# Performance work log

Hardware: AMD Instinct MI355X
Metric: run time of the kernel (lower is better)

The kernel has to match this reference:

```python
import jax, jax.numpy as jnp
import numpy as np
import math

D_MODEL = 1024
N_HEADS = 16
HEAD_DIM = D_MODEL // N_HEADS  # 64
KV_DIM = 4 * HEAD_DIM          # 256
THETA = 10000.0
B, T = 2, 2048


def setup_inputs() -> dict:
    key = jax.random.key(0)
    ks = jax.random.split(key, 14)
    s = lambda k, *sh: jax.random.normal(k, sh, dtype=jnp.float32) * 0.02
    inp = {
        "x": jax.random.normal(ks[0], (B, T, D_MODEL), dtype=jnp.float32),
        "mask": jnp.tril(jnp.ones((T, T), dtype=jnp.int32))[None, None],  # causal [1,1,T,T]
        "Wq": s(ks[1], D_MODEL, D_MODEL), "bq": jnp.zeros((D_MODEL,), jnp.float32),
        "Wkv": s(ks[2], D_MODEL, KV_DIM), "bkv": jnp.zeros((KV_DIM,), jnp.float32),
        "Wk": s(ks[3], KV_DIM, D_MODEL), "bk": jnp.zeros((D_MODEL,), jnp.float32),
        "Wv": s(ks[4], KV_DIM, D_MODEL), "bv": jnp.zeros((D_MODEL,), jnp.float32),
        "Wo": s(ks[5], D_MODEL, D_MODEL), "bo": jnp.zeros((D_MODEL,), jnp.float32),
        "Wkr": s(ks[6], HEAD_DIM, HEAD_DIM),  # decoupled k_rope linear, no bias
    }
    return inp


def _rotate_half(x):
    x1, x2 = jnp.split(x, 2, axis=-1)
    return jnp.concatenate((-x2, x1), axis=-1)


def reference(x, mask, Wq, bq, Wkv, bkv, Wk, bk, Wv, bv, Wo, bo, Wkr):
    Bq, Tq, C = x.shape
    kv = x @ Wkv + bkv                                # [B,T,KV_DIM]
    k = (kv @ Wk + bk).reshape(Bq, Tq, N_HEADS, HEAD_DIM).transpose(0, 2, 1, 3)
    v = (kv @ Wv + bv).reshape(Bq, Tq, N_HEADS, HEAD_DIM).transpose(0, 2, 1, 3)
    q = (x @ Wq + bq).reshape(Bq, Tq, N_HEADS, HEAD_DIM).transpose(0, 2, 1, 3)

    # standard RoPE on q
    inv_freq = 1.0 / (THETA ** (jnp.arange(0, HEAD_DIM, 2, dtype=jnp.float32) / HEAD_DIM))
    t = jnp.arange(Tq, dtype=jnp.float32)
    freqs = t[:, None] * inv_freq[None, :]            # [T, D/2]
    emb = jnp.concatenate((freqs, freqs), axis=-1)    # [T, D]
    q = q * jnp.cos(emb) + _rotate_half(q) * jnp.sin(emb)

    # decoupled position path for k: scale by position index, then linear
    k = (k * t[None, None, :, None]) @ Wkr            # [B,H,T,D]

    attn = jnp.einsum('bhtd,bhsd->bhts', q, k) * (1.0 / math.sqrt(HEAD_DIM))
    attn = jnp.where(mask == 0, -jnp.inf, attn)
    attn = jax.nn.softmax(attn, axis=-1)
    y = jnp.einsum('bhts,bhsd->bhtd', attn, v)
    y = y.transpose(0, 2, 1, 3).reshape(Bq, Tq, C)
    return y @ Wo + bo
```

## Files before the change

### kernel.cpp

```cpp
#include <hip/hip_runtime.h>
#include <hip/hip_bf16.h>
#include <math.h>

typedef __bf16 bf16x8 __attribute__((ext_vector_type(8)));
typedef __bf16 bf16x4 __attribute__((ext_vector_type(4)));
typedef float  f32x4  __attribute__((ext_vector_type(4)));

#define T_SEQ 2048
#define NH    16
#define HD    64
#define DM    1024
#define QSCALE 0.18033688011112043f

__device__ __forceinline__ f32x4 mfma16(bf16x8 a, bf16x8 b, f32x4 c) {
    return __builtin_amdgcn_mfma_f32_16x16x32_bf16(a, b, c, 0, 0, 0);
}

__device__ __forceinline__ void tsplit_body(const float* __restrict__ in,
                                            __bf16* __restrict__ oh, __bf16* __restrict__ ol,
                                            int K, int N, int n0, int k0, int SPLIT,
                                            float* tile )
{
    const int tid = threadIdx.x;
#pragma unroll
    for (int it = 0; it < 2; ++it) {
        int r = it * 32 + (tid >> 3), c8 = (tid & 7) * 8;
        f32x4 a0 = *(const f32x4*)&in[(size_t)(k0 + r) * N + n0 + c8];
        f32x4 a1 = *(const f32x4*)&in[(size_t)(k0 + r) * N + n0 + c8 + 4];
#pragma unroll
        for (int j = 0; j < 4; ++j) { tile[r * 65 + c8 + j] = a0[j]; tile[r * 65 + c8 + 4 + j] = a1[j]; }
    }
    __syncthreads();
    const int n = tid >> 2, kb = (tid & 3) * 16;
    bf16x8 h0, h1, l0, l1;
#pragma unroll
    for (int j = 0; j < 8; ++j) {
        float v0 = tile[(kb + j) * 65 + n], v1 = tile[(kb + 8 + j) * 65 + n];
        __bf16 hb0 = (__bf16)v0, hb1 = (__bf16)v1;
        h0[j] = hb0; h1[j] = hb1;
        if (SPLIT) { l0[j] = (__bf16)(v0 - (float)hb0); l1[j] = (__bf16)(v1 - (float)hb1); }
    }
    size_t o = (size_t)(n0 + n) * K + k0 + kb;
    *(bf16x8*)&oh[o] = h0; *(bf16x8*)&oh[o + 8] = h1;
    if (SPLIT) { *(bf16x8*)&ol[o] = l0; *(bf16x8*)&ol[o + 8] = l1; }
}

__global__ __launch_bounds__(256)
void prep(const float* __restrict__ x, const float* __restrict__ Wq,
          const float* __restrict__ Wkv, const float* __restrict__ Wv,
          const float* __restrict__ Wo, const float* __restrict__ Wk,
          const float* __restrict__ Wkr, const float* __restrict__ bk,
          __bf16* xh, __bf16* xl, __bf16* Wqt_h, __bf16* Wqt_l,
          __bf16* Wkvt_h, __bf16* Wkvt_l, __bf16* Wvt, __bf16* Wot,
          __bf16* W2th, __bf16* W2tl, float* b2)
{
    __shared__ float tile[64 * 65];
    const int g = blockIdx.x, tid = threadIdx.x;
    if (g < 2048) {
        size_t idx = ((size_t)g * 256 + tid) * 8;
        f32x4 a0 = *(const f32x4*)&x[idx];
        f32x4 a1 = *(const f32x4*)&x[idx + 4];
        bf16x8 h, l;
#pragma unroll
        for (int j = 0; j < 4; ++j) {
            __bf16 h0 = (__bf16)a0[j];
            h[j]     = h0; l[j]     = (__bf16)(a0[j] - (float)h0);
            __bf16 h1 = (__bf16)a1[j];
            h[4 + j] = h1; l[4 + j] = (__bf16)(a1[j] - (float)h1);
        }
        *(bf16x8*)&xh[idx] = h;
        *(bf16x8*)&xl[idx] = l;
    } else if (g < 2304) {
        int i = g - 2048;
        tsplit_body(Wq, Wqt_h, Wqt_l, 1024, 1024, (i & 15) * 64, (i >> 4) * 64, 1, tile);
    } else if (g < 2368) {
        int i = g - 2304;
        tsplit_body(Wkv, Wkvt_h, Wkvt_l, 1024, 256, (i & 3) * 64, (i >> 2) * 64, 1, tile);
    } else if (g < 2432) {
        int i = g - 2368;
        tsplit_body(Wv, Wvt, nullptr, 256, 1024, (i & 15) * 64, (i >> 4) * 64, 0, tile);
    } else if (g < 2688) {
        int i = g - 2432;
        tsplit_body(Wo, Wot, nullptr, 1024, 1024, (i & 15) * 64, (i >> 4) * 64, 0, tile);
    } else {
        int o    = (g - 2688) * 256 + tid;
        int rowk = o >> 10, col = o & 1023;
        int h = col >> 6, d = col & 63;
        float acc = 0.0f;
        if (rowk < 256) {
#pragma unroll 8
            for (int j = 0; j < 64; ++j)
                acc += Wk[(size_t)rowk * DM + h * HD + j] * Wkr[j * HD + d];
            __bf16 hb = (__bf16)acc;
            W2th[(size_t)col * 256 + rowk] = hb;
            W2tl[(size_t)col * 256 + rowk] = (__bf16)(acc - (float)hb);
        } else {
#pragma unroll 8
            for (int j = 0; j < 64; ++j)
                acc += bk[h * HD + j] * Wkr[j * HD + d];
            b2[col] = acc;
        }
    }
}

template <int DUALA, int DUALB, int OUTM, int EPI>
__device__ __forceinline__
void gemm_body(char* smem,
               const __bf16* __restrict__ Ahi, const __bf16* __restrict__ Alo,
               const __bf16* __restrict__ Bhi, const __bf16* __restrict__ Blo,
               const float* __restrict__ bias, void* __restrict__ Cp,
               void* __restrict__ Cp2, int m0, int n0, int N, int K)
{
    __bf16* Ah = (__bf16*)smem;
    __bf16* Al = (__bf16*)(smem + 8192);
    __bf16* Bh = (__bf16*)(smem + 16384);
    __bf16* Bl = (__bf16*)(smem + 24576);

    const int tid  = threadIdx.x;
    const int w    = tid >> 6;
    const int lane = tid & 63;
    const int l16  = lane & 15;
    const int quad = lane >> 4;
    const int wy   = w >> 1, wx = w & 1;

    f32x4 acc[4][4];
#pragma unroll
    for (int i = 0; i < 4; ++i)
#pragma unroll
        for (int j = 0; j < 4; ++j) acc[i][j] = (f32x4)0.0f;

    for (int k0 = 0; k0 < K; k0 += 32) {
        __syncthreads();
#pragma unroll
        for (int i = 0; i < 2; ++i) {
            int s = i * 256 + tid, row = s >> 2, c8 = (s & 3) * 8;
            *(bf16x8*)&Ah[row * 32 + c8] = *(const bf16x8*)&Ahi[(size_t)(m0 + row) * K + k0 + c8];
            if (DUALA)
                *(bf16x8*)&Al[row * 32 + c8] = *(const bf16x8*)&Alo[(size_t)(m0 + row) * K + k0 + c8];
            *(bf16x8*)&Bh[row * 32 + c8] = *(const bf16x8*)&Bhi[(size_t)(n0 + row) * K + k0 + c8];
            if (DUALB)
                *(bf16x8*)&Bl[row * 32 + c8] = *(const bf16x8*)&Blo[(size_t)(n0 + row) * K + k0 + c8];
        }
        __syncthreads();

        bf16x8 bfh[4], bfl[4];
#pragma unroll
        for (int ct = 0; ct < 4; ++ct) {
            bfh[ct] = *(const bf16x8*)&Bh[(wx * 64 + ct * 16 + l16) * 32 + quad * 8];
            if (DUALB) bfl[ct] = *(const bf16x8*)&Bl[(wx * 64 + ct * 16 + l16) * 32 + quad * 8];
        }
#pragma unroll
        for (int mf = 0; mf < 4; ++mf) {
            bf16x8 ah = *(const bf16x8*)&Ah[(wy * 64 + mf * 16 + l16) * 32 + quad * 8];
            bf16x8 al;
            if (DUALA) al = *(const bf16x8*)&Al[(wy * 64 + mf * 16 + l16) * 32 + quad * 8];
#pragma unroll
            for (int ct = 0; ct < 4; ++ct) {
                acc[mf][ct] = mfma16(ah, bfh[ct], acc[mf][ct]);
                if (DUALA) acc[mf][ct] = mfma16(al, bfh[ct], acc[mf][ct]);
                if (DUALB) acc[mf][ct] = mfma16(ah, bfl[ct], acc[mf][ct]);
            }
        }
    }

    float bias_v[4];
#pragma unroll
    for (int ct = 0; ct < 4; ++ct)
        bias_v[ct] = bias ? bias[n0 + wx * 64 + ct * 16 + l16] : 0.0f;

    if (EPI == 1) {
        __bf16* Chi = (__bf16*)Cp;
        __bf16* Clo = (__bf16*)Cp2;
#pragma unroll
        for (int mf = 0; mf < 4; ++mf) {
#pragma unroll
            for (int r = 0; r < 4; ++r) {
                int   m = m0 + wy * 64 + mf * 16 + quad * 4 + r;
                float t = (float)(m & (T_SEQ - 1));
#pragma unroll
                for (int ct = 0; ct < 2; ++ct) {
                    int   d   = ct * 16 + l16;
                    float inv = powf(10000.0f, -(float)d * (1.0f / 32.0f));
                    float sv, cv;
                    sincosf(t * inv, &sv, &cv);
                    float lo = acc[mf][ct][r]     + bias_v[ct];
                    float hi = acc[mf][ct + 2][r] + bias_v[ct + 2];
                    float v0 = (lo * cv - hi * sv) * QSCALE;
                    float v1 = (hi * cv + lo * sv) * QSCALE;
                    size_t i0 = (size_t)m * N + n0 + wx * 64 + d;
                    size_t i1 = i0 + 32;
                    __bf16 h0 = (__bf16)v0, h1 = (__bf16)v1;
                    Chi[i0] = h0; Clo[i0] = (__bf16)(v0 - (float)h0);
                    Chi[i1] = h1; Clo[i1] = (__bf16)(v1 - (float)h1);
                }
            }
        }
    } else if (EPI == 3) {
        __syncthreads();
        __bf16* vt = (__bf16*)(smem + w * 9216);
#pragma unroll
        for (int mf = 0; mf < 4; ++mf)
#pragma unroll
            for (int ct = 0; ct < 4; ++ct)
#pragma unroll
                for (int r = 0; r < 4; ++r)
                    vt[(ct * 16 + l16) * 72 + mf * 16 + quad * 4 + r] =
                        (__bf16)(acc[mf][ct][r] + bias_v[ct]);
        const int bb   = m0 >> 11;
        const int head = (n0 + wx * 64) >> 6;
        const int bh   = bb * 16 + head;
        __bf16* out    = (__bf16*)Cp;
        size_t  gbase  = ((size_t)(bh * 64 + lane)) * T_SEQ + (m0 & (T_SEQ - 1)) + wy * 64;
#pragma unroll
        for (int j8 = 0; j8 < 8; ++j8)
            *(bf16x8*)&out[gbase + j8 * 8] = *(const bf16x8*)&vt[lane * 72 + j8 * 8];
    } else {
#pragma unroll
        for (int mf = 0; mf < 4; ++mf) {
#pragma unroll
            for (int r = 0; r < 4; ++r) {
                int   m     = m0 + wy * 64 + mf * 16 + quad * 4 + r;
                float scale = (EPI == 2) ? (float)(m & (T_SEQ - 1)) : 1.0f;
#pragma unroll
                for (int ct = 0; ct < 4; ++ct) {
                    float  v   = (acc[mf][ct][r] + bias_v[ct]) * scale;
                    size_t idx = (size_t)m * N + n0 + wx * 64 + ct * 16 + l16;
                    if (OUTM == 1)      ((float*)Cp)[idx]  = v;
                    else if (OUTM == 0) ((__bf16*)Cp)[idx] = (__bf16)v;
                    else {
                        __bf16 hb = (__bf16)v;
                        ((__bf16*)Cp)[idx]  = hb;
                        ((__bf16*)Cp2)[idx] = (__bf16)(v - (float)hb);
                    }
                }
            }
        }
    }
}

__global__ __launch_bounds__(256)
void gemm_qkv(const __bf16* xh, const __bf16* xl,
              const __bf16* Wqt_h, const __bf16* Wqt_l, const float* bq,
              __bf16* qhi, __bf16* qlo,
              const __bf16* Wkvt_h, const __bf16* Wkvt_l, const float* bkv,
              __bf16* kvhi, __bf16* kvlo)
{
    __shared__ __attribute__((aligned(16))) char smem[36864];
    const int m0 = blockIdx.y * 128;
    if (blockIdx.x < 8)
        gemm_body<1, 1, 2, 1>(smem, xh, xl, Wqt_h, Wqt_l, bq, qhi, qlo,
                              m0, blockIdx.x * 128, 1024, 1024);
    else
        gemm_body<1, 1, 2, 0>(smem, xh, xl, Wkvt_h, Wkvt_l, bkv, kvhi, kvlo,
                              m0, (blockIdx.x - 8) * 128, 256, 1024);
}

__global__ __launch_bounds__(256)
void gemm_kv2(const __bf16* kvhi, const __bf16* kvlo,
              const __bf16* W2th, const __bf16* W2tl, const float* b2,
              __bf16* khi, __bf16* klo,
              const __bf16* Wvt, const float* bv, __bf16* vtg)
{
    __shared__ __attribute__((aligned(16))) char smem[36864];
    const int m0 = blockIdx.y * 128;
    if (blockIdx.x < 8)
        gemm_body<1, 1, 2, 2>(smem, kvhi, kvlo, W2th, W2tl, b2, khi, klo,
                              m0, blockIdx.x * 128, 1024, 256);
    else
        gemm_body<1, 0, 0, 3>(smem, kvhi, kvlo, Wvt, Wvt, bv, vtg, nullptr,
                              m0, (blockIdx.x - 8) * 128, 1024, 256);
}

__global__ __launch_bounds__(256)
void gemm_o(const __bf16* ybb, const __bf16* Wot, const float* bo, float* out)
{
    __shared__ __attribute__((aligned(16))) char smem[36864];
    gemm_body<0, 0, 1, 0>(smem, ybb, ybb, Wot, Wot, bo, out, nullptr,
                          blockIdx.y * 128, blockIdx.x * 128, 1024, 1024);
}

#define KSP 72
#define PSP 72
__global__ __launch_bounds__(256, 3)
void attn_v4(const __bf16* __restrict__ qhi, const __bf16* __restrict__ qlo,
             const __bf16* __restrict__ khi, const __bf16* __restrict__ klo,
             const __bf16* __restrict__ vtg, __bf16* __restrict__ yb)
{
    __shared__ __attribute__((aligned(16))) __bf16 Kh[64 * KSP];
    __shared__ __attribute__((aligned(16))) __bf16 Kl[64 * KSP];
    __shared__ __attribute__((aligned(16))) __bf16 Vt[64 * KSP];
    __shared__ __attribute__((aligned(16))) __bf16 Pw[4][2][16 * PSP];

    const int tid  = threadIdx.x;
    const int w    = tid >> 6;
    const int lane = tid & 63;
    const int l16  = lane & 15;
    const int quad = lane >> 4;

    const int g  = blockIdx.x;
    const int bh = g & 31, a = g >> 5;
    const int tile = (a < 8) ? (15 - 2 * a) : (2 * (a - 8));
    const int b = bh >> 4, h = bh & 15;
    const int q0 = tile * 128;

    bf16x8 qh[2][2], ql[2][2];
#pragma unroll
    for (int f = 0; f < 2; ++f) {
        const int    qrow = q0 + 64 * f + 16 * w + l16;
        const size_t qoff = (size_t)(b * T_SEQ + qrow) * DM + h * HD;
#pragma unroll
        for (int s = 0; s < 2; ++s) {
            qh[f][s] = *(const bf16x8*)&qhi[qoff + s * 32 + quad * 8];
            ql[f][s] = *(const bf16x8*)&qlo[qoff + s * 32 + quad * 8];
        }
    }

    f32x4 o[2][4];
#pragma unroll
    for (int f = 0; f < 2; ++f)
#pragma unroll
        for (int i = 0; i < 4; ++i) o[f][i] = (f32x4)0.0f;
    float m_i[2] = {-1e30f, -1e30f}, l_i[2] = {0.f, 0.f};

    const int srow = tid >> 3, sc8 = (tid & 7) * 8;

    for (int j0 = 0; j0 <= q0 + 64; j0 += 64) {
        const bool act0 = (j0 <= q0);
        __syncthreads();
#pragma unroll
        for (int it = 0; it < 2; ++it) {
            int    r  = it * 32 + srow;
            size_t gk = (size_t)(b * T_SEQ + j0 + r) * DM + h * HD + sc8;
            *(bf16x8*)&Kh[r * KSP + sc8] = *(const bf16x8*)&khi[gk];
            *(bf16x8*)&Kl[r * KSP + sc8] = *(const bf16x8*)&klo[gk];
            *(bf16x8*)&Vt[r * KSP + sc8] =
                *(const bf16x8*)&vtg[(size_t)(bh * HD + r) * T_SEQ + j0 + sc8];
        }
        __syncthreads();

        f32x4 sa[2][4];
#pragma unroll
        for (int f = 0; f < 2; ++f)
#pragma unroll
            for (int i = 0; i < 4; ++i) sa[f][i] = (f32x4)0.0f;
#pragma unroll
        for (int s = 0; s < 2; ++s) {
#pragma unroll
            for (int kc = 0; kc < 4; ++kc) {
                bf16x8 kh = *(const bf16x8*)&Kh[(kc * 16 + l16) * KSP + s * 32 + quad * 8];
                bf16x8 kv = *(const bf16x8*)&Kl[(kc * 16 + l16) * KSP + s * 32 + quad * 8];
                sa[1][kc] = mfma16(kh, qh[1][s], sa[1][kc]);
                sa[1][kc] = mfma16(kv, qh[1][s], sa[1][kc]);
                sa[1][kc] = mfma16(kh, ql[1][s], sa[1][kc]);
                if (act0) {
                    sa[0][kc] = mfma16(kh, qh[0][s], sa[0][kc]);
                    sa[0][kc] = mfma16(kv, qh[0][s], sa[0][kc]);
                    sa[0][kc] = mfma16(kh, ql[0][s], sa[0][kc]);
                }
            }
        }

#pragma unroll
        for (int f = 0; f < 2; ++f) {
            if (f == 0 && !act0) continue;
            const int  qrow = q0 + 64 * f + 16 * w + l16;
            const bool need = (j0 + 63 > q0 + 64 * f + 16 * w);
            if (need) {
#pragma unroll
                for (int kc = 0; kc < 4; ++kc)
#pragma unroll
                    for (int r = 0; r < 4; ++r)
                        if (j0 + kc * 16 + quad * 4 + r > qrow) sa[f][kc][r] = -1e30f;
            }
            float mx = -1e30f;
#pragma unroll
            for (int kc = 0; kc < 4; ++kc)
#pragma unroll
                for (int r = 0; r < 4; ++r) mx = fmaxf(mx, sa[f][kc][r]);
            mx = fmaxf(mx, __shfl_xor(mx, 16));
            mx = fmaxf(mx, __shfl_xor(mx, 32));
            float mn    = fmaxf(fmaxf(m_i[f], mx), -1e20f);
            float alpha = exp2f(m_i[f] - mn);
            m_i[f] = mn;
            float rs = 0.f;
            __bf16* pw = &Pw[w][f][0];
#pragma unroll
            for (int kc = 0; kc < 4; ++kc) {
                float p0 = exp2f(sa[f][kc][0] - mn);
                float p1 = exp2f(sa[f][kc][1] - mn);
                float p2 = exp2f(sa[f][kc][2] - mn);
                float p3 = exp2f(sa[f][kc][3] - mn);
                rs += (p0 + p1) + (p2 + p3);
                bf16x4 pk = { (__bf16)p0, (__bf16)p1, (__bf16)p2, (__bf16)p3 };
                *(bf16x4*)&pw[l16 * PSP + kc * 16 + quad * 4] = pk;
            }
            rs += __shfl_xor(rs, 16);
            rs += __shfl_xor(rs, 32);
            l_i[f] = l_i[f] * alpha + rs;
#pragma unroll
            for (int dc = 0; dc < 4; ++dc) o[f][dc] *= alpha;
        }

#pragma unroll
        for (int s = 0; s < 2; ++s) {
            bf16x8 pb1 = *(const bf16x8*)&Pw[w][1][l16 * PSP + s * 32 + quad * 8];
            bf16x8 pb0;
            if (act0) pb0 = *(const bf16x8*)&Pw[w][0][l16 * PSP + s * 32 + quad * 8];
#pragma unroll
            for (int dc = 0; dc < 4; ++dc) {
                bf16x8 va = *(const bf16x8*)&Vt[(dc * 16 + l16) * KSP + s * 32 + quad * 8];
                o[1][dc] = mfma16(va, pb1, o[1][dc]);
                if (act0) o[0][dc] = mfma16(va, pb0, o[0][dc]);
            }
        }
    }

#pragma unroll
    for (int f = 0; f < 2; ++f) {
        float   invl = 1.0f / l_i[f];
        __bf16* pw   = &Pw[w][f][0];
#pragma unroll
        for (int dc = 0; dc < 4; ++dc) {
            bf16x4 ov = { (__bf16)(o[f][dc][0] * invl), (__bf16)(o[f][dc][1] * invl),
                          (__bf16)(o[f][dc][2] * invl), (__bf16)(o[f][dc][3] * invl) };
            *(bf16x4*)&pw[l16 * PSP + dc * 16 + quad * 4] = ov;
        }
        const int qrl  = lane >> 2;
        const int dch  = (lane & 3) * 16;
        const int qrow = q0 + 64 * f + 16 * w + qrl;
        const __bf16* src = &pw[qrl * PSP + dch];
        __bf16*       dst = &yb[(size_t)(b * T_SEQ + qrow) * DM + h * HD + dch];
        *(bf16x8*)dst       = *(const bf16x8*)src;
        *(bf16x8*)(dst + 8) = *(const bf16x8*)(src + 8);
    }
}

extern "C" void kernel_launch(void* const* d_in, const int* in_sizes, int n_in,
                              void* d_out, int out_size, void* d_ws, size_t ws_size,
                              hipStream_t stream)
{
    (void)in_sizes; (void)n_in; (void)out_size; (void)ws_size;

    const float* x   = (const float*)d_in[0];
    const float* Wq  = (const float*)d_in[2];
    const float* bq  = (const float*)d_in[3];
    const float* Wkv = (const float*)d_in[4];
    const float* bkv = (const float*)d_in[5];
    const float* Wk  = (const float*)d_in[6];
    const float* bk  = (const float*)d_in[7];
    const float* Wv  = (const float*)d_in[8];
    const float* bv  = (const float*)d_in[9];
    const float* Wo  = (const float*)d_in[10];
    const float* bo  = (const float*)d_in[11];
    const float* Wkr = (const float*)d_in[12];

    const int    BT = 2 * T_SEQ;
    const size_t MB = 1024 * 1024;
    char* base = (char*)d_ws;

    __bf16* xhi    = (__bf16*)(base +  0 * MB);
    __bf16* xlo    = (__bf16*)(base +  8 * MB);
    __bf16* qhi    = (__bf16*)(base + 16 * MB);
    __bf16* qlo    = (__bf16*)(base + 24 * MB);
    __bf16* Wqt_h  = (__bf16*)(base + 32 * MB);
    __bf16* Wqt_l  = (__bf16*)(base + 34 * MB);
    __bf16* Wkvt_h = (__bf16*)(base + 36 * MB);
    __bf16* Wkvt_l = (__bf16*)(base + 37 * MB);
    __bf16* kvhi   = (__bf16*)(base + 38 * MB);
    __bf16* kvlo   = (__bf16*)(base + 40 * MB);
    __bf16* W2t_h  = (__bf16*)(base + 42 * MB);
    __bf16* W2t_l  = (__bf16*)(base + 42 * MB + 512 * 1024);
    __bf16* Wvt    = (__bf16*)(base + 43 * MB);
    __bf16* Wot    = (__bf16*)(base + 43 * MB + 512 * 1024);
    float*  b2     = (float*) (base + 45 * MB + 512 * 1024);
    __bf16* vtg    = (__bf16*)(base +  8 * MB);
    __bf16* ybb    = (__bf16*)(base +  0 * MB);
    __bf16* khi    = (__bf16*)d_out;
    __bf16* klo    = (__bf16*)d_out + (size_t)BT * DM;

    dim3 blk(256);
    prep<<<3716, blk, 0, stream>>>(x, Wq, Wkv, Wv, Wo, Wk, Wkr, bk,
                                   xhi, xlo, Wqt_h, Wqt_l, Wkvt_h, Wkvt_l,
                                   Wvt, Wot, W2t_h, W2t_l, b2);
    gemm_qkv<<<dim3(10, 32), blk, 0, stream>>>(xhi, xlo, Wqt_h, Wqt_l, bq, qhi, qlo,
                                               Wkvt_h, Wkvt_l, bkv, kvhi, kvlo);
    gemm_kv2<<<dim3(16, 32), blk, 0, stream>>>(kvhi, kvlo, W2t_h, W2t_l, b2,
                                               khi, klo, Wvt, bv, vtg);
    attn_v4<<<512, blk, 0, stream>>>(qhi, qlo, khi, klo, vtg, ybb);
    gemm_o<<<dim3(8, 32), blk, 0, stream>>>(ybb, Wot, bo, (float*)d_out);
}
```

Measured before the change: 304.1 us.

## Use direct global-to-LDS loads, regroup GEMM launches, double-buffer attention K/V tiles

GEMM tile staging now uses the global_load_lds builtin so data goes straight from global memory to LDS without passing through registers. The projection GEMMs are regrouped into three launches: kv first, then Q together with the K second-stage, then V. The attention kernel double-buffers its K/V LDS tiles and prefetches the next tile into registers while computing the current one, removing one barrier per iteration. This costs more LDS per block, and the occupancy hint drops from 3 to 2 blocks, which may reduce latency hiding.

```diff
diff --git a/kernel.cpp b/kernel.cpp
--- a/kernel.cpp
+++ b/kernel.cpp
@@ -14,6 +14,12 @@
 
 __device__ __forceinline__ f32x4 mfma16(bf16x8 a, bf16x8 b, f32x4 c) {
     return __builtin_amdgcn_mfma_f32_16x16x32_bf16(a, b, c, 0, 0, 0);
+}
+
+__device__ __forceinline__ void gl2lds(const void* g, void* l) {
+    __builtin_amdgcn_global_load_lds(
+        (const __attribute__((address_space(1))) void*)g,
+        (__attribute__((address_space(3))) void*)l, 16, 0, 0);
 }
 
 __device__ __forceinline__ void tsplit_body(const float* __restrict__ in,
@@ -134,12 +140,10 @@
 #pragma unroll
         for (int i = 0; i < 2; ++i) {
             int s = i * 256 + tid, row = s >> 2, c8 = (s & 3) * 8;
-            *(bf16x8*)&Ah[row * 32 + c8] = *(const bf16x8*)&Ahi[(size_t)(m0 + row) * K + k0 + c8];
-            if (DUALA)
-                *(bf16x8*)&Al[row * 32 + c8] = *(const bf16x8*)&Alo[(size_t)(m0 + row) * K + k0 + c8];
-            *(bf16x8*)&Bh[row * 32 + c8] = *(const bf16x8*)&Bhi[(size_t)(n0 + row) * K + k0 + c8];
-            if (DUALB)
-                *(bf16x8*)&Bl[row * 32 + c8] = *(const bf16x8*)&Blo[(size_t)(n0 + row) * K + k0 + c8];
+            gl2lds(&Ahi[(size_t)(m0 + row) * K + k0 + c8], &Ah[row * 32 + c8]);
+            if (DUALA) gl2lds(&Alo[(size_t)(m0 + row) * K + k0 + c8], &Al[row * 32 + c8]);
+            gl2lds(&Bhi[(size_t)(n0 + row) * K + k0 + c8], &Bh[row * 32 + c8]);
+            if (DUALB) gl2lds(&Blo[(size_t)(n0 + row) * K + k0 + c8], &Bl[row * 32 + c8]);
         }
         __syncthreads();
 
@@ -239,11 +243,22 @@
 }
 
 __global__ __launch_bounds__(256)
-void gemm_qkv(const __bf16* xh, const __bf16* xl,
-              const __bf16* Wqt_h, const __bf16* Wqt_l, const float* bq,
-              __bf16* qhi, __bf16* qlo,
-              const __bf16* Wkvt_h, const __bf16* Wkvt_l, const float* bkv,
-              __bf16* kvhi, __bf16* kvlo)
+void gemm_kv(const __bf16* xh, const __bf16* xl,
+             const __bf16* Wkvt_h, const __bf16* Wkvt_l, const float* bkv,
+             __bf16* kvhi, __bf16* kvlo)
+{
+    __shared__ __attribute__((aligned(16))) char smem[36864];
+    gemm_body<1, 1, 2, 0>(smem, xh, xl, Wkvt_h, Wkvt_l, bkv, kvhi, kvlo,
+                          blockIdx.y * 128, blockIdx.x * 128, 256, 1024);
+}
+
+__global__ __launch_bounds__(256)
+void gemm_qk(const __bf16* xh, const __bf16* xl,
+             const __bf16* Wqt_h, const __bf16* Wqt_l, const float* bq,
+             __bf16* qhi, __bf16* qlo,
+             const __bf16* kvhi, const __bf16* kvlo,
+             const __bf16* W2th, const __bf16* W2tl, const float* b2,
+             __bf16* khi, __bf16* klo)
 {
     __shared__ __attribute__((aligned(16))) char smem[36864];
     const int m0 = blockIdx.y * 128;
@@ -251,24 +266,17 @@
         gemm_body<1, 1, 2, 1>(smem, xh, xl, Wqt_h, Wqt_l, bq, qhi, qlo,
                               m0, blockIdx.x * 128, 1024, 1024);
     else
-        gemm_body<1, 1, 2, 0>(smem, xh, xl, Wkvt_h, Wkvt_l, bkv, kvhi, kvlo,
-                              m0, (blockIdx.x - 8) * 128, 256, 1024);
+        gemm_body<1, 1, 2, 2>(smem, kvhi, kvlo, W2th, W2tl, b2, khi, klo,
+                              m0, (blockIdx.x - 8) * 128, 1024, 256);
 }
 
 __global__ __launch_bounds__(256)
-void gemm_kv2(const __bf16* kvhi, const __bf16* kvlo,
-              const __bf16* W2th, const __bf16* W2tl, const float* b2,
-              __bf16* khi, __bf16* klo,
-              const __bf16* Wvt, const float* bv, __bf16* vtg)
+void gemm_v(const __bf16* kvhi, const __bf16* kvlo,
+            const __bf16* Wvt, const float* bv, __bf16* vtg)
 {
     __shared__ __attribute__((aligned(16))) char smem[36864];
-    const int m0 = blockIdx.y * 128;
-    if (blockIdx.x < 8)
-        gemm_body<1, 1, 2, 2>(smem, kvhi, kvlo, W2th, W2tl, b2, khi, klo,
-                              m0, blockIdx.x * 128, 1024, 256);
-    else
-        gemm_body<1, 0, 0, 3>(smem, kvhi, kvlo, Wvt, Wvt, bv, vtg, nullptr,
-                              m0, (blockIdx.x - 8) * 128, 1024, 256);
+    gemm_body<1, 0, 0, 3>(smem, kvhi, kvlo, Wvt, Wvt, bv, vtg, nullptr,
+                          blockIdx.y * 128, blockIdx.x * 128, 1024, 256);
 }
 
 __global__ __launch_bounds__(256)
@@ -281,14 +289,14 @@
 
 #define KSP 72
 #define PSP 72
-__global__ __launch_bounds__(256, 3)
-void attn_v4(const __bf16* __restrict__ qhi, const __bf16* __restrict__ qlo,
+__global__ __launch_bounds__(256, 2)
+void attn_v5(const __bf16* __restrict__ qhi, const __bf16* __restrict__ qlo,
              const __bf16* __restrict__ khi, const __bf16* __restrict__ klo,
              const __bf16* __restrict__ vtg, __bf16* __restrict__ yb)
 {
-    __shared__ __attribute__((aligned(16))) __bf16 Kh[64 * KSP];
-    __shared__ __attribute__((aligned(16))) __bf16 Kl[64 * KSP];
-    __shared__ __attribute__((aligned(16))) __bf16 Vt[64 * KSP];
+    __shared__ __attribute__((aligned(16))) __bf16 Kh2[2][64 * KSP];
+    __shared__ __attribute__((aligned(16))) __bf16 Kl2[2][64 * KSP];
+    __shared__ __attribute__((aligned(16))) __bf16 Vt2[2][64 * KSP];
     __shared__ __attribute__((aligned(16))) __bf16 Pw[4][2][16 * PSP];
 
     const int tid  = threadIdx.x;
@@ -323,20 +331,45 @@
     float m_i[2] = {-1e30f, -1e30f}, l_i[2] = {0.f, 0.f};
 
     const int srow = tid >> 3, sc8 = (tid & 7) * 8;
-
-    for (int j0 = 0; j0 <= q0 + 64; j0 += 64) {
+    bf16x8 kr[2], lr[2], vr[2];
+
+#pragma unroll
+    for (int it = 0; it < 2; ++it) {
+        int    r  = it * 32 + srow;
+        size_t gk = (size_t)(b * T_SEQ + r) * DM + h * HD + sc8;
+        kr[it] = *(const bf16x8*)&khi[gk];
+        lr[it] = *(const bf16x8*)&klo[gk];
+        vr[it] = *(const bf16x8*)&vtg[(size_t)(bh * HD + r) * T_SEQ + sc8];
+    }
+#pragma unroll
+    for (int it = 0; it < 2; ++it) {
+        int r = it * 32 + srow;
+        *(bf16x8*)&Kh2[0][r * KSP + sc8] = kr[it];
+        *(bf16x8*)&Kl2[0][r * KSP + sc8] = lr[it];
+        *(bf16x8*)&Vt2[0][r * KSP + sc8] = vr[it];
+    }
+
+    const int jmax = q0 + 64;
+    for (int j0 = 0; j0 <= jmax; j0 += 64) {
+        const int  cur  = (j0 >> 6) & 1;
         const bool act0 = (j0 <= q0);
+        const bool pre  = (j0 + 64 <= jmax);
         __syncthreads();
-#pragma unroll
-        for (int it = 0; it < 2; ++it) {
-            int    r  = it * 32 + srow;
-            size_t gk = (size_t)(b * T_SEQ + j0 + r) * DM + h * HD + sc8;
-            *(bf16x8*)&Kh[r * KSP + sc8] = *(const bf16x8*)&khi[gk];
-            *(bf16x8*)&Kl[r * KSP + sc8] = *(const bf16x8*)&klo[gk];
-            *(bf16x8*)&Vt[r * KSP + sc8] =
-                *(const bf16x8*)&vtg[(size_t)(bh * HD + r) * T_SEQ + j0 + sc8];
-        }
-        __syncthreads();
+
+        if (pre) {
+#pragma unroll
+            for (int it = 0; it < 2; ++it) {
+                int    r  = it * 32 + srow;
+                size_t gk = (size_t)(b * T_SEQ + j0 + 64 + r) * DM + h * HD + sc8;
+                kr[it] = *(const bf16x8*)&khi[gk];
+                lr[it] = *(const bf16x8*)&klo[gk];
+                vr[it] = *(const bf16x8*)&vtg[(size_t)(bh * HD + r) * T_SEQ + j0 + 64 + sc8];
+            }
+        }
+
+        const __bf16* Kh = Kh2[cur];
+        const __bf16* Kl = Kl2[cur];
+        const __bf16* Vt = Vt2[cur];
 
         f32x4 sa[2][4];
 #pragma unroll
@@ -411,6 +444,19 @@
                 bf16x8 va = *(const bf16x8*)&Vt[(dc * 16 + l16) * KSP + s * 32 + quad * 8];
                 o[1][dc] = mfma16(va, pb1, o[1][dc]);
                 if (act0) o[0][dc] = mfma16(va, pb0, o[0][dc]);
+            }
+        }
+
+        if (pre) {
+            __bf16* nKh = Kh2[cur ^ 1];
+            __bf16* nKl = Kl2[cur ^ 1];
+            __bf16* nVt = Vt2[cur ^ 1];
+#pragma unroll
+            for (int it = 0; it < 2; ++it) {
+                int r = it * 32 + srow;
+                *(bf16x8*)&nKh[r * KSP + sc8] = kr[it];
+                *(bf16x8*)&nKl[r * KSP + sc8] = lr[it];
+                *(bf16x8*)&nVt[r * KSP + sc8] = vr[it];
             }
         }
     }
@@ -482,10 +528,10 @@
     prep<<<3716, blk, 0, stream>>>(x, Wq, Wkv, Wv, Wo, Wk, Wkr, bk,
                                    xhi, xlo, Wqt_h, Wqt_l, Wkvt_h, Wkvt_l,
                                    Wvt, Wot, W2t_h, W2t_l, b2);
-    gemm_qkv<<<dim3(10, 32), blk, 0, stream>>>(xhi, xlo, Wqt_h, Wqt_l, bq, qhi, qlo,
-                                               Wkvt_h, Wkvt_l, bkv, kvhi, kvlo);
-    gemm_kv2<<<dim3(16, 32), blk, 0, stream>>>(kvhi, kvlo, W2t_h, W2t_l, b2,
-                                               khi, klo, Wvt, bv, vtg);
-    attn_v4<<<512, blk, 0, stream>>>(qhi, qlo, khi, klo, vtg, ybb);
+    gemm_kv<<<dim3(2, 32), blk, 0, stream>>>(xhi, xlo, Wkvt_h, Wkvt_l, bkv, kvhi, kvlo);
+    gemm_qk<<<dim3(16, 32), blk, 0, stream>>>(xhi, xlo, Wqt_h, Wqt_l, bq, qhi, qlo,
+                                              kvhi, kvlo, W2t_h, W2t_l, b2, khi, klo);
+    gemm_v<<<dim3(8, 32), blk, 0, stream>>>(kvhi, kvlo, Wvt, bv, vtg);
+    attn_v5<<<512, blk, 0, stream>>>(qhi, qlo, khi, klo, vtg, ybb);
     gemm_o<<<dim3(8, 32), blk, 0, stream>>>(ybb, Wot, bo, (float*)d_out);
 }
```

After: 325.6 us. +7.1%, slower.
